# Optimization experiments

Measured on AMD Instinct MI355X. Metric: run time of the kernel, lower is better.

The kernel has to match this reference:

```python
import jax, jax.numpy as jnp
import numpy as np

B, S, D, H = 2, 2048, 1024, 16
DH = D // H


def setup_inputs() -> dict:
    key = jax.random.key(0)
    ks = jax.random.split(key, 5)
    scale = 1.0 / np.sqrt(D)
    return {
        "x": jax.random.normal(ks[0], (B, S, D), dtype=jnp.float32),
        "Wq": jax.random.normal(ks[1], (D, D), dtype=jnp.float32) * scale,
        "bq": jnp.zeros((D,), jnp.float32),
        "Wk": jax.random.normal(ks[2], (D, D), dtype=jnp.float32) * scale,
        "bk": jnp.zeros((D,), jnp.float32),
        "Wv": jax.random.normal(ks[3], (D, D), dtype=jnp.float32) * scale,
        "bv": jnp.zeros((D,), jnp.float32),
        "Wo": jax.random.normal(ks[4], (D, D), dtype=jnp.float32) * scale,
        "bo": jnp.zeros((D,), jnp.float32),
    }


def reference(x, Wq, bq, Wk, bk, Wv, bv, Wo, bo):
    b, s, d = x.shape
    # QKV projections (torch Linear: x @ W.T + b)
    q = (x @ Wq.T + bq).reshape(b, s, H, DH).transpose(0, 2, 1, 3)  # [b,h,s,dh]
    k = (x @ Wk.T + bk).reshape(b, s, H, DH).transpose(0, 2, 1, 3)
    v = (x @ Wv.T + bv).reshape(b, s, H, DH).transpose(0, 2, 1, 3)
    scale = 1.0 / jnp.sqrt(jnp.array(DH, dtype=jnp.float32))
    energy = jnp.einsum("bhqd,bhkd->bhqk", q, k) * scale  # [b,h,s,s]
    attn = jax.nn.softmax(energy, axis=-1)
    out = jnp.einsum("bhqk,bhkd->bhqd", attn, v)  # [b,h,s,dh]
    out = out.transpose(0, 2, 1, 3).reshape(b, s, d)
    return out @ Wo.T + bo
```

## Files before the change

### kernel.cpp

```cpp
#include <hip/hip_runtime.h>

using bf16x8 = __attribute__((ext_vector_type(8))) short;
using f32x4  = __attribute__((ext_vector_type(4))) float;
using u32x2  = __attribute__((ext_vector_type(2))) unsigned int;

__device__ __forceinline__ unsigned short f2bf(float f) {
  union { float f; unsigned int u; } v; v.f = f;
  unsigned int u = v.u;
  unsigned int r = (u + 0x7FFFu + ((u >> 16) & 1u)) >> 16;
  return (unsigned short)r;
}

__device__ __forceinline__ unsigned int pk2bf(float a, float b) {
  union { float f; unsigned int u; } x, y; x.f = a; y.f = b;
  unsigned int ua = x.u + 0x7FFFu + ((x.u >> 16) & 1u);
  unsigned int ub = y.u + 0x7FFFu + ((y.u >> 16) & 1u);
  return __builtin_amdgcn_perm(ub, ua, 0x07060302u);
}

__device__ __forceinline__ void gl_lds16(const void* g, void* l) {
  __builtin_amdgcn_global_load_lds(
      (const __attribute__((address_space(1))) void*)g,
      (__attribute__((address_space(3))) void*)l, 16, 0, 0);
}

__global__ void cast_all(const float* __restrict__ x,
                         const float* __restrict__ wq, const float* __restrict__ wk,
                         const float* __restrict__ wv, const float* __restrict__ wo,
                         unsigned short* __restrict__ xb,
                         unsigned short* __restrict__ wqb, unsigned short* __restrict__ wkb,
                         unsigned short* __restrict__ wvb, unsigned short* __restrict__ wob) {
  size_t i4 = ((size_t)blockIdx.x * 256 + threadIdx.x) * 4;
  const float* src; unsigned short* dst; size_t off;
  if (i4 < 4194304) { src = x; dst = xb; off = i4; }
  else {
    size_t j = i4 - 4194304;
    int w = (int)(j >> 20);
    off = j & 1048575;
    src = (w == 0) ? wq : (w == 1) ? wk : (w == 2) ? wv : wo;
    dst = (w == 0) ? wqb : (w == 1) ? wkb : (w == 2) ? wvb : wob;
  }
  float4 v = *(const float4*)(src + off);
  ushort4 o;
  o.x = f2bf(v.x); o.y = f2bf(v.y); o.z = f2bf(v.z); o.w = f2bf(v.w);
  *(ushort4*)(dst + off) = o;
}

template <int BN>
__device__ __forceinline__ void gemm_tile_nt(const unsigned short* __restrict__ A,
                                             const unsigned short* __restrict__ Bm,
                                             int tile_m, int tile_n,
                                             f32x4 acc[4][BN / 32]) {
  constexpr int JN = BN / 32;
  __shared__ __align__(16) unsigned short As[128 * 32];
  __shared__ __align__(16) unsigned short Bs[BN * 32];
  const int tid = threadIdx.x;
  const int lane = tid & 63, wave = tid >> 6;
  const int quad = lane >> 4, l16 = lane & 15;
  const int wm = (wave & 1) * 64, wn = (wave >> 1) * (BN / 2);
  const int srow = tid >> 2;
  const int scol = (tid & 3) * 8;

#pragma unroll
  for (int i = 0; i < 4; i++)
#pragma unroll
    for (int j = 0; j < JN; j++)
#pragma unroll
      for (int r = 0; r < 4; r++) acc[i][j][r] = 0.f;

  for (int k0 = 0; k0 < 1024; k0 += 32) {
#pragma unroll
    for (int t = 0; t < 2; t++)
      gl_lds16(A + (size_t)(tile_m + t * 64 + srow) * 1024 + k0 + scol,
               (char*)As + t * 4096 + tid * 16);
    if (BN == 128) {
#pragma unroll
      for (int t = 0; t < 2; t++)
        gl_lds16(Bm + (size_t)(tile_n + t * 64 + srow) * 1024 + k0 + scol,
                 (char*)Bs + t * 4096 + tid * 16);
    } else {
      gl_lds16(Bm + (size_t)(tile_n + srow) * 1024 + k0 + scol, (char*)Bs + tid * 16);
    }
    __syncthreads();
    bf16x8 a[4], b[JN];
#pragma unroll
    for (int i = 0; i < 4; i++)
      a[i] = *(const bf16x8*)((const char*)As + ((wm + i * 16 + l16) * 32 + quad * 8) * 2);
#pragma unroll
    for (int j = 0; j < JN; j++)
      b[j] = *(const bf16x8*)((const char*)Bs + ((wn + j * 16 + l16) * 32 + quad * 8) * 2);
#pragma unroll
    for (int i = 0; i < 4; i++)
#pragma unroll
      for (int j = 0; j < JN; j++)
        acc[i][j] = __builtin_amdgcn_mfma_f32_16x16x32_bf16(a[i], b[j], acc[i][j], 0, 0, 0);
    __syncthreads();
  }
}

__global__ __launch_bounds__(256) void gemm_qkv(
    const unsigned short* __restrict__ xb,
    const unsigned short* __restrict__ wqb, const unsigned short* __restrict__ wkb,
    const unsigned short* __restrict__ wvb,
    const float* __restrict__ bq, const float* __restrict__ bk, const float* __restrict__ bv,
    unsigned short* __restrict__ Qo, unsigned short* __restrict__ Ko,
    unsigned short* __restrict__ Vt) {
  const int z = blockIdx.z;
  const unsigned short* Bm = (z == 0) ? wqb : (z == 1) ? wkb : wvb;
  const float* bias = (z == 0) ? bq : (z == 1) ? bk : bv;
  const int tile_m = blockIdx.y * 128, tile_n = blockIdx.x * 128;
  f32x4 acc[4][4];
  gemm_tile_nt<128>(xb, Bm, tile_m, tile_n, acc);

  const int tid = threadIdx.x, lane = tid & 63, wave = tid >> 6;
  const int quad = lane >> 4, l16 = lane & 15;
  const int wm = (wave & 1) * 64, wn = (wave >> 1) * 64;
  const float scale = (z == 0) ? 0.125f : 1.0f;

  if (z < 2) {
    unsigned short* out = (z == 0) ? Qo : Ko;
#pragma unroll
    for (int i = 0; i < 4; i++)
#pragma unroll
      for (int j = 0; j < 4; j++) {
        int n = tile_n + wn + j * 16 + l16;
        float bn = bias[n];
#pragma unroll
        for (int r = 0; r < 4; r++) {
          int m = tile_m + wm + i * 16 + quad * 4 + r;
          out[(size_t)m * 1024 + n] = f2bf((acc[i][j][r] + bn) * scale);
        }
      }
  } else {
#pragma unroll
    for (int i = 0; i < 4; i++)
#pragma unroll
      for (int j = 0; j < 4; j++) {
        int n = tile_n + wn + j * 16 + l16;
        int hh = n >> 6, dh = n & 63;
        float bn = bias[n];
        int m0 = tile_m + wm + i * 16 + quad * 4;
        int b = m0 >> 11, s = m0 & 2047;
        ushort4 pk;
        pk.x = f2bf(acc[i][j][0] + bn);
        pk.y = f2bf(acc[i][j][1] + bn);
        pk.z = f2bf(acc[i][j][2] + bn);
        pk.w = f2bf(acc[i][j][3] + bn);
        *(ushort4*)(Vt + ((size_t)((b * 16 + hh) * 64 + dh)) * 2048 + s) = pk;
      }
  }
}

__global__ __launch_bounds__(256, 2) void flash_attn(
    const unsigned short* __restrict__ Qg, const unsigned short* __restrict__ Kg,
    const unsigned short* __restrict__ Vt, unsigned short* __restrict__ AO) {
  __shared__ __align__(16) unsigned short Kl[8 * 128 * 8];
  __shared__ __align__(16) unsigned short Vl[16 * 64 * 8];
  __shared__ __align__(16) unsigned short Pl[4 * 32 * 136];

  const int tid = threadIdx.x, lane = tid & 63, wave = tid >> 6;
  const int quad = lane >> 4, l16 = lane & 15;
  const int bi = blockIdx.x;
  const int bh = (bi & 7) * 4 + ((bi >> 3) & 3);
  const int qt = bi >> 5;
  const int b = bh >> 4, h = bh & 15;
  unsigned short* Pw = Pl + wave * (32 * 136);

  const size_t qbase = ((size_t)(b * 2048 + qt * 128 + wave * 32)) * 1024 + h * 64;
  bf16x8 qf[2][2];
#pragma unroll
  for (int qs = 0; qs < 2; qs++)
#pragma unroll
    for (int ks = 0; ks < 2; ks++)
      qf[qs][ks] = *(const bf16x8*)(Qg + qbase + (size_t)(qs * 16 + l16) * 1024 +
                                    ks * 32 + quad * 8);

  f32x4 O[2][4];
  float lp[2] = {0.f, 0.f};
#pragma unroll
  for (int qs = 0; qs < 2; qs++)
#pragma unroll
    for (int mb = 0; mb < 4; mb++)
#pragma unroll
      for (int r = 0; r < 4; r++) O[qs][mb][r] = 0.f;

  for (int kt = 0; kt < 16; kt++) {
    __syncthreads();
    const size_t krow0 = (size_t)(b * 2048 + kt * 128);
#pragma unroll
    for (int t = 0; t < 4; t++) {
      int i = t * 256 + tid; int g = i >> 7, row = i & 127;
      gl_lds16(Kg + (krow0 + row) * 1024 + h * 64 + g * 8, (char*)Kl + i * 16);
    }
    const size_t vbase = ((size_t)bh * 64) * 2048 + (size_t)kt * 128;
#pragma unroll
    for (int t = 0; t < 4; t++) {
      int i = t * 256 + tid; int g = i >> 6, d = i & 63;
      gl_lds16(Vt + vbase + (size_t)d * 2048 + g * 8, (char*)Vl + i * 16);
    }
    __syncthreads();

    f32x4 sacc[2][8];
#pragma unroll
    for (int qs = 0; qs < 2; qs++)
#pragma unroll
      for (int nb = 0; nb < 8; nb++)
#pragma unroll
        for (int r = 0; r < 4; r++) sacc[qs][nb][r] = 0.f;
#pragma unroll
    for (int nb = 0; nb < 8; nb++) {
      bf16x8 kf0 = *(const bf16x8*)((const char*)Kl + ((quad) * 128 + nb * 16 + l16) * 16);
      bf16x8 kf1 = *(const bf16x8*)((const char*)Kl + ((4 + quad) * 128 + nb * 16 + l16) * 16);
#pragma unroll
      for (int qs = 0; qs < 2; qs++) {
        sacc[qs][nb] = __builtin_amdgcn_mfma_f32_16x16x32_bf16(kf0, qf[qs][0], sacc[qs][nb], 0, 0, 0);
        sacc[qs][nb] = __builtin_amdgcn_mfma_f32_16x16x32_bf16(kf1, qf[qs][1], sacc[qs][nb], 0, 0, 0);
      }
    }

#pragma unroll
    for (int qs = 0; qs < 2; qs++) {
#pragma unroll
      for (int nb = 0; nb < 8; nb++) {
        float p0 = __expf(sacc[qs][nb][0]);
        float p1 = __expf(sacc[qs][nb][1]);
        float p2 = __expf(sacc[qs][nb][2]);
        float p3 = __expf(sacc[qs][nb][3]);
        lp[qs] += (p0 + p1) + (p2 + p3);
        u32x2 d; d[0] = pk2bf(p0, p1); d[1] = pk2bf(p2, p3);
        *(u32x2*)(Pw + (qs * 16 + l16) * 136 + nb * 16 + quad * 4) = d;
      }
    }

#pragma unroll
    for (int kc = 0; kc < 4; kc++) {
      bf16x8 pf[2];
#pragma unroll
      for (int qs = 0; qs < 2; qs++)
        pf[qs] = *(const bf16x8*)(Pw + (qs * 16 + l16) * 136 + kc * 32 + quad * 8);
#pragma unroll
      for (int mb = 0; mb < 4; mb++) {
        bf16x8 vf = *(const bf16x8*)((const char*)Vl + ((kc * 4 + quad) * 64 + mb * 16 + l16) * 16);
#pragma unroll
        for (int qs = 0; qs < 2; qs++)
          O[qs][mb] = __builtin_amdgcn_mfma_f32_16x16x32_bf16(vf, pf[qs], O[qs][mb], 0, 0, 0);
      }
    }
  }

  float inv[2];
#pragma unroll
  for (int qs = 0; qs < 2; qs++) {
    float l = lp[qs];
    l += __shfl_xor(l, 16);
    l += __shfl_xor(l, 32);
    inv[qs] = 1.f / l;
  }

#pragma unroll
  for (int qs = 0; qs < 2; qs++)
#pragma unroll
    for (int mb = 0; mb < 4; mb++) {
      float o0 = O[qs][mb][0] * inv[qs];
      float o1 = O[qs][mb][1] * inv[qs];
      float o2 = O[qs][mb][2] * inv[qs];
      float o3 = O[qs][mb][3] * inv[qs];
      u32x2 d; d[0] = pk2bf(o0, o1); d[1] = pk2bf(o2, o3);
      *(u32x2*)(Pw + (qs * 16 + l16) * 72 + mb * 16 + quad * 4) = d;
    }
  const size_t orow0 = (size_t)(b * 2048 + qt * 128 + wave * 32);
#pragma unroll
  for (int p = 0; p < 4; p++) {
    int q = p * 8 + (lane >> 3), dh = (lane & 7) * 8;
    bf16x8 o = *(const bf16x8*)(Pw + q * 72 + dh);
    *(bf16x8*)(AO + (orow0 + q) * 1024 + h * 64 + dh) = o;
  }
}

__global__ __launch_bounds__(256) void gemm_out(
    const unsigned short* __restrict__ AO, const unsigned short* __restrict__ wob,
    const float* __restrict__ bo, float* __restrict__ out) {
  const int tile_m = blockIdx.y * 128, tile_n = blockIdx.x * 64;
  f32x4 acc[4][2];
  gemm_tile_nt<64>(AO, wob, tile_m, tile_n, acc);
  const int tid = threadIdx.x, lane = tid & 63, wave = tid >> 6;
  const int quad = lane >> 4, l16 = lane & 15;
  const int wm = (wave & 1) * 64, wn = (wave >> 1) * 32;
#pragma unroll
  for (int i = 0; i < 4; i++)
#pragma unroll
    for (int j = 0; j < 2; j++) {
      int n = tile_n + wn + j * 16 + l16;
      float bn = bo[n];
#pragma unroll
      for (int r = 0; r < 4; r++) {
        int m = tile_m + wm + i * 16 + quad * 4 + r;
        out[(size_t)m * 1024 + n] = acc[i][j][r] + bn;
      }
    }
}

extern "C" void kernel_launch(void* const* d_in, const int* in_sizes, int n_in,
                              void* d_out, int out_size, void* d_ws, size_t ws_size,
                              hipStream_t stream) {
  (void)in_sizes; (void)n_in; (void)out_size; (void)ws_size;
  const float* x  = (const float*)d_in[0];
  const float* Wq = (const float*)d_in[1];
  const float* bq = (const float*)d_in[2];
  const float* Wk = (const float*)d_in[3];
  const float* bk = (const float*)d_in[4];
  const float* Wv = (const float*)d_in[5];
  const float* bv = (const float*)d_in[6];
  const float* Wo = (const float*)d_in[7];
  const float* bo = (const float*)d_in[8];
  float* out = (float*)d_out;

  char* ws = (char*)d_ws;
  unsigned short* xb  = (unsigned short*)(ws + 0);
  unsigned short* wqb = (unsigned short*)(ws + 8388608);
  unsigned short* wkb = (unsigned short*)(ws + 10485760);
  unsigned short* wvb = (unsigned short*)(ws + 12582912);
  unsigned short* wob = (unsigned short*)(ws + 14680064);
  unsigned short* Qb  = (unsigned short*)(ws + 16777216);
  unsigned short* Kb  = (unsigned short*)(ws + 25165824);
  unsigned short* Vtb = (unsigned short*)(ws + 33554432);
  unsigned short* AOb = (unsigned short*)(ws + 41943040);

  cast_all<<<8192, 256, 0, stream>>>(x, Wq, Wk, Wv, Wo, xb, wqb, wkb, wvb, wob);
  gemm_qkv<<<dim3(8, 32, 3), dim3(256), 0, stream>>>(xb, wqb, wkb, wvb, bq, bk, bv, Qb, Kb, Vtb);
  flash_attn<<<512, 256, 0, stream>>>(Qb, Kb, Vtb, AOb);
  gemm_out<<<dim3(16, 32, 1), dim3(256), 0, stream>>>(AOb, wob, bo, out);
}
```

Before: 222.9 us.

## Restructure flash attention per query subtile with exp2, smaller P buffer, higher occupancy

Folds log2(e) into the Q scale so the softmax uses the native exp2 instruction, and replaces round-to-nearest bf16 packing of P with truncation. The score/softmax/PV loop now runs one 16-row query subtile at a time, which halves the live score registers and shrinks the per-wave P LDS buffer to a swizzled 16x128 layout. Launch bounds rise to 3 blocks per CU. This lowers register and LDS pressure and the cost of exp, at the price of less MFMA interleaving across subtiles and truncated P precision.

```diff
diff --git a/kernel.cpp b/kernel.cpp
--- a/kernel.cpp
+++ b/kernel.cpp
@@ -16,6 +16,19 @@
   unsigned int ua = x.u + 0x7FFFu + ((x.u >> 16) & 1u);
   unsigned int ub = y.u + 0x7FFFu + ((y.u >> 16) & 1u);
   return __builtin_amdgcn_perm(ub, ua, 0x07060302u);
+}
+
+__device__ __forceinline__ unsigned int pk2bf_trunc(float a, float b) {
+  union { float f; unsigned int u; } x, y; x.f = a; y.f = b;
+  return __builtin_amdgcn_perm(y.u, x.u, 0x07060302u);
+}
+
+__device__ __forceinline__ float fast_exp2(float x) {
+#if __has_builtin(__builtin_amdgcn_exp2f)
+  return __builtin_amdgcn_exp2f(x);
+#else
+  return exp2f(x);
+#endif
 }
 
 __device__ __forceinline__ void gl_lds16(const void* g, void* l) {
@@ -115,7 +128,7 @@
   const int tid = threadIdx.x, lane = tid & 63, wave = tid >> 6;
   const int quad = lane >> 4, l16 = lane & 15;
   const int wm = (wave & 1) * 64, wn = (wave >> 1) * 64;
-  const float scale = (z == 0) ? 0.125f : 1.0f;
+  const float scale = (z == 0) ? 0.18033688011112042f : 1.0f;
 
   if (z < 2) {
     unsigned short* out = (z == 0) ? Qo : Ko;
@@ -151,12 +164,12 @@
   }
 }
 
-__global__ __launch_bounds__(256, 2) void flash_attn(
+__global__ __launch_bounds__(256, 3) void flash_attn(
     const unsigned short* __restrict__ Qg, const unsigned short* __restrict__ Kg,
     const unsigned short* __restrict__ Vt, unsigned short* __restrict__ AO) {
   __shared__ __align__(16) unsigned short Kl[8 * 128 * 8];
   __shared__ __align__(16) unsigned short Vl[16 * 64 * 8];
-  __shared__ __align__(16) unsigned short Pl[4 * 32 * 136];
+  __shared__ __align__(16) unsigned short Pl[4 * 16 * 16 * 8];
 
   const int tid = threadIdx.x, lane = tid & 63, wave = tid >> 6;
   const int quad = lane >> 4, l16 = lane & 15;
@@ -164,7 +177,7 @@
   const int bh = (bi & 7) * 4 + ((bi >> 3) & 3);
   const int qt = bi >> 5;
   const int b = bh >> 4, h = bh & 15;
-  unsigned short* Pw = Pl + wave * (32 * 136);
+  unsigned short* Pw = Pl + wave * 2048;
 
   const size_t qbase = ((size_t)(b * 2048 + qt * 128 + wave * 32)) * 1024 + h * 64;
   bf16x8 qf[2][2];
@@ -200,50 +213,40 @@
     }
     __syncthreads();
 
-    f32x4 sacc[2][8];
-#pragma unroll
-    for (int qs = 0; qs < 2; qs++)
+#pragma unroll
+    for (int qs = 0; qs < 2; qs++) {
+      f32x4 sacc[8];
 #pragma unroll
       for (int nb = 0; nb < 8; nb++)
 #pragma unroll
-        for (int r = 0; r < 4; r++) sacc[qs][nb][r] = 0.f;
-#pragma unroll
-    for (int nb = 0; nb < 8; nb++) {
-      bf16x8 kf0 = *(const bf16x8*)((const char*)Kl + ((quad) * 128 + nb * 16 + l16) * 16);
-      bf16x8 kf1 = *(const bf16x8*)((const char*)Kl + ((4 + quad) * 128 + nb * 16 + l16) * 16);
-#pragma unroll
-      for (int qs = 0; qs < 2; qs++) {
-        sacc[qs][nb] = __builtin_amdgcn_mfma_f32_16x16x32_bf16(kf0, qf[qs][0], sacc[qs][nb], 0, 0, 0);
-        sacc[qs][nb] = __builtin_amdgcn_mfma_f32_16x16x32_bf16(kf1, qf[qs][1], sacc[qs][nb], 0, 0, 0);
-      }
-    }
-
-#pragma unroll
-    for (int qs = 0; qs < 2; qs++) {
+        for (int r = 0; r < 4; r++) sacc[nb][r] = 0.f;
 #pragma unroll
       for (int nb = 0; nb < 8; nb++) {
-        float p0 = __expf(sacc[qs][nb][0]);
-        float p1 = __expf(sacc[qs][nb][1]);
-        float p2 = __expf(sacc[qs][nb][2]);
-        float p3 = __expf(sacc[qs][nb][3]);
+        bf16x8 kf0 = *(const bf16x8*)((const char*)Kl + ((quad) * 128 + nb * 16 + l16) * 16);
+        bf16x8 kf1 = *(const bf16x8*)((const char*)Kl + ((4 + quad) * 128 + nb * 16 + l16) * 16);
+        sacc[nb] = __builtin_amdgcn_mfma_f32_16x16x32_bf16(kf0, qf[qs][0], sacc[nb], 0, 0, 0);
+        sacc[nb] = __builtin_amdgcn_mfma_f32_16x16x32_bf16(kf1, qf[qs][1], sacc[nb], 0, 0, 0);
+      }
+
+#pragma unroll
+      for (int nb = 0; nb < 8; nb++) {
+        float p0 = fast_exp2(sacc[nb][0]);
+        float p1 = fast_exp2(sacc[nb][1]);
+        float p2 = fast_exp2(sacc[nb][2]);
+        float p3 = fast_exp2(sacc[nb][3]);
         lp[qs] += (p0 + p1) + (p2 + p3);
-        u32x2 d; d[0] = pk2bf(p0, p1); d[1] = pk2bf(p2, p3);
-        *(u32x2*)(Pw + (qs * 16 + l16) * 136 + nb * 16 + quad * 4) = d;
-      }
-    }
-
-#pragma unroll
-    for (int kc = 0; kc < 4; kc++) {
-      bf16x8 pf[2];
-#pragma unroll
-      for (int qs = 0; qs < 2; qs++)
-        pf[qs] = *(const bf16x8*)(Pw + (qs * 16 + l16) * 136 + kc * 32 + quad * 8);
-#pragma unroll
-      for (int mb = 0; mb < 4; mb++) {
-        bf16x8 vf = *(const bf16x8*)((const char*)Vl + ((kc * 4 + quad) * 64 + mb * 16 + l16) * 16);
-#pragma unroll
-        for (int qs = 0; qs < 2; qs++)
-          O[qs][mb] = __builtin_amdgcn_mfma_f32_16x16x32_bf16(vf, pf[qs], O[qs][mb], 0, 0, 0);
+        u32x2 d; d[0] = pk2bf_trunc(p0, p1); d[1] = pk2bf_trunc(p2, p3);
+        *(u32x2*)(Pw + (2 * nb + (quad >> 1)) * 128 + l16 * 8 + (quad & 1) * 4) = d;
+      }
+
+#pragma unroll
+      for (int kc = 0; kc < 4; kc++) {
+        bf16x8 pf = *(const bf16x8*)(Pw + (kc * 4 + quad) * 128 + l16 * 8);
+#pragma unroll
+        for (int mb = 0; mb < 4; mb++) {
+          bf16x8 vf = *(const bf16x8*)((const char*)Vl + ((kc * 4 + quad) * 64 + mb * 16 + l16) * 16);
+          O[qs][mb] = __builtin_amdgcn_mfma_f32_16x16x32_bf16(vf, pf, O[qs][mb], 0, 0, 0);
+        }
       }
     }
   }
@@ -257,8 +260,9 @@
     inv[qs] = 1.f / l;
   }
 
-#pragma unroll
-  for (int qs = 0; qs < 2; qs++)
+  const size_t orow0 = (size_t)(b * 2048 + qt * 128 + wave * 32);
+#pragma unroll
+  for (int qs = 0; qs < 2; qs++) {
 #pragma unroll
     for (int mb = 0; mb < 4; mb++) {
       float o0 = O[qs][mb][0] * inv[qs];
@@ -266,14 +270,14 @@
       float o2 = O[qs][mb][2] * inv[qs];
       float o3 = O[qs][mb][3] * inv[qs];
       u32x2 d; d[0] = pk2bf(o0, o1); d[1] = pk2bf(o2, o3);
-      *(u32x2*)(Pw + (qs * 16 + l16) * 72 + mb * 16 + quad * 4) = d;
-    }
-  const size_t orow0 = (size_t)(b * 2048 + qt * 128 + wave * 32);
-#pragma unroll
-  for (int p = 0; p < 4; p++) {
-    int q = p * 8 + (lane >> 3), dh = (lane & 7) * 8;
-    bf16x8 o = *(const bf16x8*)(Pw + q * 72 + dh);
-    *(bf16x8*)(AO + (orow0 + q) * 1024 + h * 64 + dh) = o;
+      *(u32x2*)(Pw + (2 * mb + (quad >> 1)) * 128 + l16 * 8 + (quad & 1) * 4) = d;
+    }
+#pragma unroll
+    for (int t = 0; t < 2; t++) {
+      int q = t * 8 + (lane >> 3), dh = (lane & 7) * 8;
+      bf16x8 o = *(const bf16x8*)(Pw + (lane & 7) * 128 + q * 8);
+      *(bf16x8*)(AO + (orow0 + qs * 16 + q) * 1024 + h * 64 + dh) = o;
+    }
   }
 }
 
```

New measurement: 249.3 us. 11.9% more time.
